# Performance work log

Measured on AMD Instinct MI355X. Metric: run time of the kernel, lower is better.

Reference implementation:

```python
import jax, jax.numpy as jnp
import numpy as np
from jax import lax

L_STEPS = 10
MU = 0.1
GAUSS_KS = 51
GAUSS_SIGMA = 6.0
LEAKY_SLOPE = 0.01

# normalized sobel kernels (kornia normalized=True divides by sum(|k|)=8)
KX = jnp.array([[-1., 0., 1.], [-2., 0., 2.], [-1., 0., 1.]]) / 8.0
KY = KX.T


def _depthwise_valid(x, k2d):
    # x: [B,C,h,w] (already padded), k2d: [kh,kw]; cross-correlation per channel
    C = x.shape[1]
    kern = jnp.broadcast_to(k2d, (C, 1) + k2d.shape).astype(x.dtype)
    return lax.conv_general_dilated(x, kern, (1, 1), 'VALID',
                                    feature_group_count=C,
                                    dimension_numbers=('NCHW', 'OIHW', 'NCHW'))


def spatial_gradient(img):
    # img [B,1,h,w] -> [B,1,2,h,w] (dx, dy), replicate border like kornia
    p = jnp.pad(img, ((0, 0), (0, 0), (1, 1), (1, 1)), mode='edge')
    gx = _depthwise_valid(p, KX)
    gy = _depthwise_valid(p, KY)
    return jnp.stack([gx, gy], axis=2)


def _gauss1d(ks, sigma):
    x = jnp.arange(ks, dtype=jnp.float32) - (ks - 1) / 2.0
    g = jnp.exp(-0.5 * (x / sigma) ** 2)
    return g / jnp.sum(g)


def gaussian_blur(x):
    # border_type='constant' -> zero pad, separable depthwise blur
    g = _gauss1d(GAUSS_KS, GAUSS_SIGMA)
    p = GAUSS_KS // 2
    xp = jnp.pad(x, ((0, 0), (0, 0), (p, p), (p, p)))
    y = _depthwise_valid(xp, g[:, None])   # blur along H
    return _depthwise_valid(y, g[None, :])  # blur along W


def conv3x3(x, w, b=None):
    y = lax.conv_general_dilated(x, w, (1, 1), [(1, 1), (1, 1)],
                                 dimension_numbers=('NCHW', 'OIHW', 'NCHW'))
    if b is not None:
        y = y + b[None, :, None, None]
    return y


def res_block_apply(z, I, w1, b1, w2):
    x = jnp.concatenate([z, I], axis=1)          # [B,2,h,w]
    x = conv3x3(x, w1, b1)                        # [B,100,h,w]
    x = jnp.where(x > 0, x, LEAKY_SLOPE * x)
    return conv3x3(x, w2)                         # [B,1,h,w]


def deform_image(img, grid):
    # img [B,C,h,w], grid [B,h,w,2] pixel (x,y); bilinear with border clamp
    B, C, h, w = img.shape
    x, y = grid[..., 0], grid[..., 1]
    x0f, y0f = jnp.floor(x), jnp.floor(y)
    wx, wy = x - x0f, y - y0f
    x0 = jnp.clip(x0f.astype(jnp.int32), 0, w - 1)
    x1 = jnp.clip(x0f.astype(jnp.int32) + 1, 0, w - 1)
    y0 = jnp.clip(y0f.astype(jnp.int32), 0, h - 1)
    y1 = jnp.clip(y0f.astype(jnp.int32) + 1, 0, h - 1)
    bidx = jnp.arange(B)[:, None, None]
    Ia = img[bidx, :, y0, x0]  # [B,h,w,C]
    Ib = img[bidx, :, y0, x1]
    Ic = img[bidx, :, y1, x0]
    Id = img[bidx, :, y1, x1]
    wa = ((1 - wx) * (1 - wy))[..., None]
    wb = (wx * (1 - wy))[..., None]
    wc = ((1 - wx) * wy)[..., None]
    wd = (wx * wy)[..., None]
    out = wa * Ia + wb * Ib + wc * Ic + wd * Id
    return out.transpose(0, 3, 1, 2)


def _id_grid(h, w, dtype):
    xs = jnp.arange(w, dtype=dtype)
    ys = jnp.arange(h, dtype=dtype)
    gx, gy = jnp.meshgrid(xs, ys, indexing='xy')
    return jnp.stack([gx, gy], axis=-1)[None]  # [1,h,w,2] (x,y) pixel coords


def setup_inputs() -> dict:
    key = jax.random.key(0)
    ks = jax.random.split(key, 5)
    B, h, w = 4, 256, 256
    source = jax.random.normal(ks[0], (B, 1, h, w), jnp.float32)
    z0 = 0.1 * jax.random.normal(ks[1], (1, 1, h, w), jnp.float32)
    conv1_w = jax.random.normal(ks[2], (L_STEPS, 100, 2, 3, 3), jnp.float32) / np.sqrt(2 * 9)
    conv1_b = 0.01 * jax.random.normal(ks[3], (L_STEPS, 100), jnp.float32)
    conv2_w = jax.random.normal(ks[4], (L_STEPS, 1, 100, 3, 3), jnp.float32) / np.sqrt(100 * 9)
    return {"source": source, "z0": z0, "conv1_w": conv1_w,
            "conv1_b": conv1_b, "conv2_w": conv2_w}


def reference(source, z0, conv1_w, conv1_b, conv2_w):
    B, _, h, w = source.shape
    l = L_STEPS
    id_grid = _id_grid(h, w, source.dtype)
    z = jnp.broadcast_to(z0, (B,) + z0.shape[1:])
    images, residuals, fields, grads = [source], [z], [], []
    for i in range(l):
        g = spatial_gradient(images[i])                       # [B,1,2,h,w]
        grads.append(g)
        field = gaussian_blur(-residuals[i] * g[:, 0])        # [B,2,h,w]
        field = field.transpose(0, 2, 3, 1)                   # [B,h,w,2]
        fields.append(field)
        f = res_block_apply(residuals[i], images[i],
                            conv1_w[i], conv1_b[i], conv2_w[i]) / l
        z_next = residuals[i] + f
        residuals.append(z_next)
        deformation = id_grid - field / l
        images.append(deform_image(images[i], deformation)
                      + z_next * (MU ** 2) / l)
    return (jnp.stack(images), jnp.stack(fields),
            jnp.stack(residuals), jnp.stack(grads))
```

## Files before the change

kernel.cpp:

```cpp
#include <hip/hip_runtime.h>
#include <hip/hip_bf16.h>
#include <math.h>

#define B 4
#define H 256
#define W 256
#define HW 65536
#define BHW (B * HW)
#define LSTEPS 10
#define NCH 100
#define KS 51
#define KR 25

typedef __fp16 h2 __attribute__((ext_vector_type(2)));
typedef __fp16 half8 __attribute__((ext_vector_type(8)));
typedef float f32x4 __attribute__((ext_vector_type(4)));
typedef unsigned u32x4v __attribute__((ext_vector_type(4)));
typedef unsigned u32x2v __attribute__((ext_vector_type(2)));

static __device__ __forceinline__ h2 pack_f16(float a, float b) {
#if __has_builtin(__builtin_amdgcn_cvt_pkrtz)
    return __builtin_amdgcn_cvt_pkrtz(a, b);
#else
    h2 r; r.x = (__fp16)a; r.y = (__fp16)b; return r;
#endif
}
static __device__ __forceinline__ unsigned packu(float a, float b) {
    return __builtin_bit_cast(unsigned, pack_f16(a, b));
}

__global__ void init_kernel(const float* __restrict__ src, const float* __restrict__ z0,
                            const float* __restrict__ conv1_w, const float* __restrict__ conv1_b,
                            const float* __restrict__ conv2_w,
                            float* __restrict__ images0, float* __restrict__ res0,
                            unsigned* __restrict__ gwpk,
                            unsigned* __restrict__ a1, unsigned* __restrict__ a2) {
    int tid = blockIdx.x * 256 + threadIdx.x;
    images0[tid] = src[tid];
    res0[tid] = z0[tid & (HW - 1)];
    if (tid == 0) {
        float e[KS];
        float s = 0.f;
        for (int k = 0; k < KS; k++) {
            float x = (float)(k - KR) / 6.0f;
            e[k] = expf(-0.5f * x * x);
            s += e[k];
        }
        for (int k = 0; k < KS; k++) {
            float g = e[k] / s;
            gwpk[k] = packu(g, g);
        }
    }
    if (tid < LSTEPS * 112) {
        int i = tid / 112, c = tid % 112;
        unsigned* dst = a1 + (size_t)tid * 16;
        if (c < NCH) {
            const float* wz = conv1_w + ((size_t)i * NCH + c) * 18;
            float bias = conv1_b[(size_t)i * NCH + c];
#pragma unroll
            for (int t = 0; t < 9; t++) dst[t] = packu(wz[t], wz[9 + t]);
            dst[9] = packu(bias, 0.f);
#pragma unroll
            for (int t = 10; t < 16; t++) dst[t] = 0u;
        } else {
#pragma unroll
            for (int t = 0; t < 16; t++) dst[t] = 0u;
        }
    }
    if (tid >= 4096 && tid < 4096 + LSTEPS * 16) {
        int r = tid - 4096;
        int i = r / 16, q = r % 16;
        unsigned* dst = a2 + (size_t)r * 64;
        for (int cp = 0; cp < 64; cp++) {
            int c0 = 2 * cp, c1 = 2 * cp + 1;
            float f0 = (q < 9 && c0 < NCH) ? conv2_w[((size_t)i * NCH + c0) * 9 + q] : 0.f;
            float f1 = (q < 9 && c1 < NCH) ? conv2_w[((size_t)i * NCH + c1) * 9 + q] : 0.f;
            dst[cp] = packu(f0, f1);
        }
    }
}

__global__ __launch_bounds__(256, 4) void mfma_smap_kernel(
        const float* __restrict__ z, const float* __restrict__ img,
        const unsigned* __restrict__ a1, const unsigned* __restrict__ a2,
        __hip_bfloat16* __restrict__ S,
        float* __restrict__ grads_i, unsigned* __restrict__ t01) {
    __shared__ unsigned feat_l[256 * 16];
    __shared__ unsigned h_l[64 * 64];
    __shared__ float zrow[3][W + 2];
    __shared__ float irow[3][W + 2];
    int bid = blockIdx.x;
    int b = bid >> 8, y = bid & 255;
    int x = threadIdx.x;
    int p = y * W + x;
    const float* zp = z + (b << 16);
    const float* ip = img + (b << 16);

    bool rv0, rv1, rv2;
#pragma unroll
    for (int r = 0; r < 3; r++) {
        int yy = y - 1 + r;
        bool rv = ((unsigned)yy < (unsigned)H);
        int yc = min(max(yy, 0), H - 1);
        zrow[r][x + 1] = rv ? zp[yc * W + x] : 0.f;
        irow[r][x + 1] = ip[yc * W + x];
        if (x == 0) {
            zrow[r][0] = 0.f;       zrow[r][W + 1] = 0.f;
            irow[r][0] = ip[yc * W + 0];
            irow[r][W + 1] = ip[yc * W + (W - 1)];
        }
        if (r == 0) rv0 = rv; else if (r == 1) rv1 = rv; else rv2 = rv;
    }
    __syncthreads();

    float ir[9], zv9[9];
#pragma unroll
    for (int r = 0; r < 3; r++)
#pragma unroll
        for (int c = 0; c < 3; c++) {
            ir[r * 3 + c] = irow[r][x + c];
            zv9[r * 3 + c] = zrow[r][x + c];
        }
    float gx = ((ir[2] + 2.f * ir[5] + ir[8]) - (ir[0] + 2.f * ir[3] + ir[6])) * 0.125f;
    float gy = ((ir[6] + 2.f * ir[7] + ir[8]) - (ir[0] + 2.f * ir[1] + ir[2])) * 0.125f;
    grads_i[(b * 2 + 0) * HW + p] = gx;
    grads_i[(b * 2 + 1) * HW + p] = gy;
    float zc = zv9[4];
    t01[(b << 16) + p] = packu(-zc * gx, -zc * gy);

    unsigned fd[16];
#pragma unroll
    for (int r = 0; r < 3; r++) {
        bool rv = (r == 0) ? rv0 : (r == 1) ? rv1 : rv2;
#pragma unroll
        for (int c = 0; c < 3; c++) {
            int k = r * 3 + c;
            bool ok = rv && ((unsigned)(x + c - 1) < (unsigned)W);
            float iv = ok ? ir[k] : 0.f;
            fd[k] = packu(zv9[k], iv);
        }
    }
    fd[9] = packu(1.0f, 0.f);
#pragma unroll
    for (int k = 10; k < 16; k++) fd[k] = 0u;

    {
        unsigned base = (unsigned)(x * 16);
        unsigned swzf = (unsigned)((x & 3) << 2);
#pragma unroll
        for (int g = 0; g < 4; g++) {
            u32x4v v = {fd[g * 4], fd[g * 4 + 1], fd[g * 4 + 2], fd[g * 4 + 3]};
            *(u32x4v*)(feat_l + base + ((unsigned)(g * 4) ^ swzf)) = v;
        }
    }
    if (x < 64) {
        unsigned swz0 = (unsigned)((x & 15) << 2);
        u32x4v zv = {0u, 0u, 0u, 0u};
        *(u32x4v*)(h_l + x * 64 + (56u ^ swz0)) = zv;
        *(u32x4v*)(h_l + x * 64 + (60u ^ swz0)) = zv;
    }

    int w = threadIdx.x >> 6;
    int lane = threadIdx.x & 63;
    int l15 = lane & 15, lg = lane >> 4;

    half8 A1f[7];
#pragma unroll
    for (int mt = 0; mt < 7; mt++)
        A1f[mt] = __builtin_bit_cast(half8,
            *(const u32x4v*)(a1 + (size_t)((mt * 16 + l15) * 16 + lg * 4)));
    half8 A2f[4];
#pragma unroll
    for (int ks = 0; ks < 4; ks++)
        A2f[ks] = __builtin_bit_cast(half8,
            *(const u32x4v*)(a2 + (size_t)(l15 * 64 + ks * 16 + lg * 4)));

    __syncthreads();

    unsigned hrow = (unsigned)((w * 16 + l15) * 64);
    unsigned swz = (unsigned)(l15 << 2);
    unsigned fswz = (unsigned)((l15 & 3) << 2);

#pragma unroll
    for (int qt = 0; qt < 4; qt++) {
        int pxq = qt * 64 + w * 16;
        half8 B1f = __builtin_bit_cast(half8,
            *(const u32x4v*)(feat_l + (unsigned)((pxq + l15) * 16) + ((unsigned)(lg * 4) ^ fswz)));
        f32x4 zero4 = {0.f, 0.f, 0.f, 0.f};
        f32x4 acc[7];
#pragma unroll
        for (int mt = 0; mt < 7; mt++)
            acc[mt] = __builtin_amdgcn_mfma_f32_16x16x32_f16(A1f[mt], B1f, zero4, 0, 0, 0);
#pragma unroll
        for (int mt = 0; mt < 7; mt++) {
            float l0 = fmaxf(acc[mt][0], 0.01f * acc[mt][0]);
            float l1 = fmaxf(acc[mt][1], 0.01f * acc[mt][1]);
            float l2 = fmaxf(acc[mt][2], 0.01f * acc[mt][2]);
            float l3 = fmaxf(acc[mt][3], 0.01f * acc[mt][3]);
            u32x2v dv = {packu(l0, l1), packu(l2, l3)};
            unsigned c = (unsigned)(mt * 8 + lg * 2);
            *(u32x2v*)(h_l + hrow + (c ^ swz)) = dv;
        }
        f32x4 acc2 = {0.f, 0.f, 0.f, 0.f};
#pragma unroll
        for (int ks = 0; ks < 4; ks++) {
            half8 B2f = __builtin_bit_cast(half8,
                *(const u32x4v*)(h_l + hrow + ((unsigned)(ks * 16 + lg * 4) ^ swz)));
            acc2 = __builtin_amdgcn_mfma_f32_16x16x32_f16(A2f[ks], B2f, acc2, 0, 0, 0);
        }
        int xg = pxq + l15;
        size_t sbase = (size_t)(b << 16) + (size_t)y * W + xg;
#pragma unroll
        for (int r = 0; r < 4; r++) {
            int q = lg * 4 + r;
            if (q < 9) S[(size_t)q * BHW + sbase] = __float2bfloat16(acc2[r]);
        }
    }
}

__global__ void vhblur_deform_kernel(const unsigned* __restrict__ t01g,
                                     const unsigned* __restrict__ gwpk,
                                     float* __restrict__ fields_i,
                                     const float* __restrict__ img, const float* __restrict__ z,
                                     const __hip_bfloat16* __restrict__ S,
                                     float* __restrict__ res_next, float* __restrict__ img_next) {
    int b = blockIdx.x >> 8;
    int row = blockIdx.x & 255;
    __shared__ unsigned s01[W + 2 * KR];
    int x = threadIdx.x;

    const unsigned* t01 = t01g + (b << 16);
    h2 vacc[3];
#pragma unroll
    for (int j = 0; j < 3; j++) { h2 zz = {(__fp16)0.f, (__fp16)0.f}; vacc[j] = zz; }
#pragma unroll
    for (int k = 0; k < KS; k++) {
        int rr = row - KR + k;
        if ((unsigned)rr < (unsigned)H) {
            h2 tv = __builtin_bit_cast(h2, t01[rr * W + x]);
            h2 wv = __builtin_bit_cast(h2, gwpk[k]);
            vacc[k % 3] = wv * tv + vacc[k % 3];
        }
    }
    h2 v01 = vacc[0] + vacc[1] + vacc[2];
    s01[KR + x] = __builtin_bit_cast(unsigned, v01);
    if (x < KR) s01[x] = 0u;
    else if (x >= W - KR) s01[x + 2 * KR] = 0u;
    __syncthreads();

    h2 hacc[3];
#pragma unroll
    for (int j = 0; j < 3; j++) { h2 zz = {(__fp16)0.f, (__fp16)0.f}; hacc[j] = zz; }
#pragma unroll
    for (int k = 0; k < KS; k++) {
        h2 sv = __builtin_bit_cast(h2, s01[x + k]);
        h2 wv = __builtin_bit_cast(h2, gwpk[k]);
        hacc[k % 3] = wv * sv + hacc[k % 3];
    }
    h2 a01 = hacc[0] + hacc[1] + hacc[2];
    float a0 = (float)a01.x, a1v = (float)a01.y;

    int p = row * W + x;
    int tid = (b << 16) + p;
    float2* fdst = (float2*)(fields_i + (size_t)tid * 2);
    *fdst = make_float2(a0, a1v);

    float f = 0.f;
#pragma unroll
    for (int q = 0; q < 9; q++) {
        int yy = row - 1 + q / 3;
        int xx = x - 1 + q % 3;
        if (((unsigned)yy < (unsigned)H) && ((unsigned)xx < (unsigned)W))
            f += __bfloat162float(S[(size_t)q * BHW + (b << 16) + yy * W + xx]);
    }
    float zn = z[tid] + f / 10.0f;
    res_next[tid] = zn;

    float sx = (float)x - a0 / 10.0f;
    float sy = (float)row - a1v / 10.0f;
    float x0f = floorf(sx), y0f = floorf(sy);
    float wx = sx - x0f, wy = sy - y0f;
    int ix0 = min(max((int)x0f, 0), W - 1);
    int ix1 = min(max((int)x0f + 1, 0), W - 1);
    int iy0 = min(max((int)y0f, 0), H - 1);
    int iy1 = min(max((int)y0f + 1, 0), H - 1);
    const float* im = img + (b << 16);
    float Ia = im[iy0 * W + ix0], Ib = im[iy0 * W + ix1];
    float Ic = im[iy1 * W + ix0], Id = im[iy1 * W + ix1];
    float out = (1.f - wx) * (1.f - wy) * Ia + wx * (1.f - wy) * Ib
              + (1.f - wx) * wy * Ic + wx * wy * Id;
    img_next[tid] = out + zn * 0.001f;
}

extern "C" void kernel_launch(void* const* d_in, const int* in_sizes, int n_in,
                              void* d_out, int out_size, void* d_ws, size_t ws_size,
                              hipStream_t stream) {
    const float* source  = (const float*)d_in[0];
    const float* z0      = (const float*)d_in[1];
    const float* conv1_w = (const float*)d_in[2];
    const float* conv1_b = (const float*)d_in[3];
    const float* conv2_w = (const float*)d_in[4];

    float* out = (float*)d_out;
    float* images    = out;
    float* fields    = images + (size_t)11 * B * HW;
    float* residuals = fields + (size_t)10 * B * HW * 2;
    float* grads     = residuals + (size_t)11 * B * HW;

    unsigned* t01 = (unsigned*)d_ws;
    __hip_bfloat16* S = (__hip_bfloat16*)(t01 + (size_t)BHW);
    unsigned* gwpk = (unsigned*)(S + (size_t)9 * BHW);
    unsigned* a1 = gwpk + 64;
    unsigned* a2 = a1 + (size_t)LSTEPS * 112 * 16;

    init_kernel<<<BHW / 256, 256, 0, stream>>>(source, z0, conv1_w, conv1_b, conv2_w,
                                               images, residuals, gwpk, a1, a2);

    for (int i = 0; i < LSTEPS; i++) {
        const float* img_i = images + (size_t)i * B * HW;
        const float* z_i   = residuals + (size_t)i * B * HW;
        float* fields_i    = fields + (size_t)i * B * HW * 2;

        mfma_smap_kernel<<<B * H, 256, 0, stream>>>(z_i, img_i,
                a1 + (size_t)i * 112 * 16, a2 + (size_t)i * 16 * 64, S,
                grads + (size_t)i * B * 2 * HW, t01);
        vhblur_deform_kernel<<<B * H, 256, 0, stream>>>(t01, gwpk, fields_i,
                img_i, z_i, S,
                residuals + (size_t)(i + 1) * B * HW, images + (size_t)(i + 1) * B * HW);
    }
}
```

Before: 279.2 us.

## Stage blur input rows in shared memory and process four rows per block

The vertical Gaussian pass now loads a 54-row tile of the packed t01 input into LDS once per block and computes four output rows per 1024-thread block, where before each 256-thread block read 51 rows from global memory for a single row. This removes the repeated global and L2 reads of overlapping rows. In exchange, each block uses about 55KB of LDS, there are fewer and larger blocks (256 instead of 1024), and launch_bounds(1024,1) limits occupancy, so latency hiding may suffer.

```diff
diff --git a/kernel.cpp b/kernel.cpp
--- a/kernel.cpp
+++ b/kernel.cpp
@@ -218,34 +218,42 @@
     }
 }
 
-__global__ void vhblur_deform_kernel(const unsigned* __restrict__ t01g,
-                                     const unsigned* __restrict__ gwpk,
-                                     float* __restrict__ fields_i,
-                                     const float* __restrict__ img, const float* __restrict__ z,
-                                     const __hip_bfloat16* __restrict__ S,
-                                     float* __restrict__ res_next, float* __restrict__ img_next) {
-    int b = blockIdx.x >> 8;
-    int row = blockIdx.x & 255;
-    __shared__ unsigned s01[W + 2 * KR];
-    int x = threadIdx.x;
-
+__global__ __launch_bounds__(1024, 1) void vhblur_deform_kernel(
+        const unsigned* __restrict__ t01g,
+        const unsigned* __restrict__ gwpk,
+        float* __restrict__ fields_i,
+        const float* __restrict__ img, const float* __restrict__ z,
+        const __hip_bfloat16* __restrict__ S,
+        float* __restrict__ res_next, float* __restrict__ img_next) {
+    __shared__ unsigned st[54][W];
+    __shared__ unsigned hs[4][W + 2 * KR];
+    int bid = blockIdx.x;
+    int b = bid >> 6;
+    int y0 = (bid & 63) << 2;
+    int tid = threadIdx.x;
+    int r = tid >> 8;
+    int x = tid & 255;
     const unsigned* t01 = t01g + (b << 16);
+
+    for (int j = r; j < 54; j += 4) {
+        int rr = y0 - KR + j;
+        st[j][x] = ((unsigned)rr < (unsigned)H) ? t01[rr * W + x] : 0u;
+    }
+    __syncthreads();
+
     h2 vacc[3];
 #pragma unroll
     for (int j = 0; j < 3; j++) { h2 zz = {(__fp16)0.f, (__fp16)0.f}; vacc[j] = zz; }
 #pragma unroll
     for (int k = 0; k < KS; k++) {
-        int rr = row - KR + k;
-        if ((unsigned)rr < (unsigned)H) {
-            h2 tv = __builtin_bit_cast(h2, t01[rr * W + x]);
-            h2 wv = __builtin_bit_cast(h2, gwpk[k]);
-            vacc[k % 3] = wv * tv + vacc[k % 3];
-        }
+        h2 tv = __builtin_bit_cast(h2, st[r + k][x]);
+        h2 wv = __builtin_bit_cast(h2, gwpk[k]);
+        vacc[k % 3] = wv * tv + vacc[k % 3];
     }
     h2 v01 = vacc[0] + vacc[1] + vacc[2];
-    s01[KR + x] = __builtin_bit_cast(unsigned, v01);
-    if (x < KR) s01[x] = 0u;
-    else if (x >= W - KR) s01[x + 2 * KR] = 0u;
+    hs[r][KR + x] = __builtin_bit_cast(unsigned, v01);
+    if (x < KR) hs[r][x] = 0u;
+    else if (x >= W - KR) hs[r][x + 2 * KR] = 0u;
     __syncthreads();
 
     h2 hacc[3];
@@ -253,31 +261,32 @@
     for (int j = 0; j < 3; j++) { h2 zz = {(__fp16)0.f, (__fp16)0.f}; hacc[j] = zz; }
 #pragma unroll
     for (int k = 0; k < KS; k++) {
-        h2 sv = __builtin_bit_cast(h2, s01[x + k]);
+        h2 sv = __builtin_bit_cast(h2, hs[r][x + k]);
         h2 wv = __builtin_bit_cast(h2, gwpk[k]);
         hacc[k % 3] = wv * sv + hacc[k % 3];
     }
     h2 a01 = hacc[0] + hacc[1] + hacc[2];
     float a0 = (float)a01.x, a1v = (float)a01.y;
 
-    int p = row * W + x;
-    int tid = (b << 16) + p;
-    float2* fdst = (float2*)(fields_i + (size_t)tid * 2);
+    int y = y0 + r;
+    int p = y * W + x;
+    int gtid = (b << 16) + p;
+    float2* fdst = (float2*)(fields_i + (size_t)gtid * 2);
     *fdst = make_float2(a0, a1v);
 
     float f = 0.f;
 #pragma unroll
     for (int q = 0; q < 9; q++) {
-        int yy = row - 1 + q / 3;
+        int yy = y - 1 + q / 3;
         int xx = x - 1 + q % 3;
         if (((unsigned)yy < (unsigned)H) && ((unsigned)xx < (unsigned)W))
             f += __bfloat162float(S[(size_t)q * BHW + (b << 16) + yy * W + xx]);
     }
-    float zn = z[tid] + f / 10.0f;
-    res_next[tid] = zn;
+    float zn = z[gtid] + f / 10.0f;
+    res_next[gtid] = zn;
 
     float sx = (float)x - a0 / 10.0f;
-    float sy = (float)row - a1v / 10.0f;
+    float sy = (float)y - a1v / 10.0f;
     float x0f = floorf(sx), y0f = floorf(sy);
     float wx = sx - x0f, wy = sy - y0f;
     int ix0 = min(max((int)x0f, 0), W - 1);
@@ -289,7 +298,7 @@
     float Ic = im[iy1 * W + ix0], Id = im[iy1 * W + ix1];
     float out = (1.f - wx) * (1.f - wy) * Ia + wx * (1.f - wy) * Ib
               + (1.f - wx) * wy * Ic + wx * wy * Id;
-    img_next[tid] = out + zn * 0.001f;
+    img_next[gtid] = out + zn * 0.001f;
 }
 
 extern "C" void kernel_launch(void* const* d_in, const int* in_sizes, int n_in,
@@ -324,7 +333,7 @@
         mfma_smap_kernel<<<B * H, 256, 0, stream>>>(z_i, img_i,
                 a1 + (size_t)i * 112 * 16, a2 + (size_t)i * 16 * 64, S,
                 grads + (size_t)i * B * 2 * HW, t01);
-        vhblur_deform_kernel<<<B * H, 256, 0, stream>>>(t01, gwpk, fields_i,
+        vhblur_deform_kernel<<<B * H / 4, 1024, 0, stream>>>(t01, gwpk, fields_i,
                 img_i, z_i, S,
                 residuals + (size_t)(i + 1) * B * HW, images + (size_t)(i + 1) * B * HW);
     }
```

After: 253.0 us. -9.4%, faster.
